# Kernel optimization log

Hardware: AMD Instinct MI355X
Metric: run time of the kernel (lower is better)

## Reference

```python
import jax, jax.numpy as jnp
import numpy as np

WIN = 7            # skimage default win_size
K1 = 0.01
K2 = 0.03
DATA_RANGE = 1.0   # images are in [0, 1]
PAD = (WIN - 1) // 2


def _uniform_filter_valid(x):
    # x: [N, 1, H, W] -> valid 7x7 box filter (== skimage uniform_filter cropped by PAD)
    k = jnp.ones((1, 1, WIN, WIN), x.dtype) / (WIN * WIN)
    return jax.lax.conv_general_dilated(
        x, k, window_strides=(1, 1), padding='VALID',
        dimension_numbers=('NCHW', 'OIHW', 'NCHW'))


def _ssim_mean(a, b):
    # a, b: [B, C, H, W]; each [H, W] slice is one independent SSIM image
    B, C, H, W = a.shape
    x = a.reshape(B * C, 1, H, W)
    y = b.reshape(B * C, 1, H, W)

    ux = _uniform_filter_valid(x)
    uy = _uniform_filter_valid(y)
    uxx = _uniform_filter_valid(x * x)
    uyy = _uniform_filter_valid(y * y)
    uxy = _uniform_filter_valid(x * y)

    NP = WIN * WIN
    cov_norm = NP / (NP - 1.0)  # sample covariance correction (skimage default)
    vx = cov_norm * (uxx - ux * ux)
    vy = cov_norm * (uyy - uy * uy)
    vxy = cov_norm * (uxy - ux * uy)

    C1 = (K1 * DATA_RANGE) ** 2
    C2 = (K2 * DATA_RANGE) ** 2

    S = ((2.0 * ux * uy + C1) * (2.0 * vxy + C2)) / \
        ((ux * ux + uy * uy + C1) * (vx + vy + C2))

    # skimage crops PAD border then means; VALID conv already cropped it.
    # All images are the same size, so np.average(per-image means) == global mean.
    return jnp.mean(S)


def setup_inputs() -> dict:
    key = jax.random.key(0)
    k1, k2 = jax.random.split(key)
    pred = jax.random.uniform(k1, (32, 4, 384, 384), dtype=jnp.float32)
    actual = jax.random.uniform(k2, (32, 4, 384, 384), dtype=jnp.float32)
    return {"pred": pred, "actual": actual}


def reference(pred, actual):
    return _ssim_mean(pred, actual)
```

## Files before the change

kernel.cpp:

```cpp
#include <hip/hip_runtime.h>


#define H 384
#define W 384
#define IMGSZ (H * W)
#define OWIDTH 378
#define NIMG 128
#define NCT 7
#define NRS 6
#define WPI (NCT * NRS)
#define NBLK (NIMG * WPI)
#define P4 65
#define CH 8

__device__ __forceinline__ float wave_reduce(float v) {
#pragma unroll
    for (int off = 32; off > 0; off >>= 1) v += __shfl_down(v, off, 64);
    return v;
}

#define VST(SN, SO, LR, XN, YN) do {                                      \
    const float xo = xv[SO], yo = yv[SO];                                 \
    const float xn = (XN), yn = (YN);                                     \
    sx += xn - xo; sy += yn - yo;                                         \
    sq = fmaf(xn, xn, fmaf(yn, yn, fmaf(-xo, xo, fmaf(-yo, yo, sq))));    \
    sxy = fmaf(xn, yn, fmaf(-xo, yo, sxy));                               \
    xv[SN] = xn; yv[SN] = yn;                                             \
    st[(LR) * P4 + t] = make_float4(sx, sy, sq, sxy);                     \
} while (0)

__global__ __launch_bounds__(64, 4) void ssim_main(const float* __restrict__ pred,
                                                   const float* __restrict__ act,
                                                   float* __restrict__ partials) {
    __shared__ __align__(16) float4 st[CH * P4 + 5];

    const int t = threadIdx.x;
    const int wid = blockIdx.x;
    const int img = wid / WPI;
    const int rem = wid - img * WPI;
    const int rs = rem / NCT;
    const int ct = rem - rs * NCT;

    const int c0 = ct * 58;
    const bool last_rs = (rs == NRS - 1);
    const int y0 = last_rs ? (H - 70) : rs * 64;
    const int ylo = last_rs ? 6 : 0;
    const int nc_raw = OWIDTH - c0;
    const int ncols = (nc_raw < 58) ? nc_raw : 58;

    int col = c0 + t;
    col = (col < W) ? col : (W - 1);
    const float* px = pred + (size_t)img * IMGSZ + (size_t)y0 * W + col;
    const float* py = act  + (size_t)img * IMGSZ + (size_t)y0 * W + col;

    float xv[8], yv[8];
    float pfx[7], pfy[7];
#pragma unroll
    for (int i = 0; i < 7; ++i) { xv[i] = px[i * W]; yv[i] = py[i * W]; }
#pragma unroll
    for (int i = 0; i < 7; ++i) { pfx[i] = px[(7 + i) * W]; pfy[i] = py[(7 + i) * W]; }
    float sx = 0.f, sy = 0.f, sq = 0.f, sxy = 0.f;
#pragma unroll
    for (int i = 0; i < 7; ++i) {
        sx += xv[i]; sy += yv[i];
        sq = fmaf(xv[i], xv[i], fmaf(yv[i], yv[i], sq));
        sxy = fmaf(xv[i], yv[i], sxy);
    }
    st[t] = make_float4(sx, sy, sq, sxy);
    VST(7, 0, 1, pfx[0], pfy[0]);
    VST(0, 1, 2, pfx[1], pfy[1]);
    VST(1, 2, 3, pfx[2], pfy[2]);
    VST(2, 3, 4, pfx[3], pfy[3]);
    VST(3, 4, 5, pfx[4], pfy[4]);
    VST(4, 5, 6, pfx[5], pfy[5]);
    VST(5, 6, 7, pfx[6], pfy[6]);

    const int r = t >> 3;
    const int k = t & 7;
    const int nmax = ncols - 8 * k;
    const float4* qbase = st + r * P4 + 8 * k;
    const float C1B = 0.2401f;
    const float C2B = 2.1168f;
    float acc = 0.f;

    for (int c = 0; c < 8; ++c) {
        float nfx[8], nfy[8];
        if (c < 7) {
#pragma unroll
            for (int i = 0; i < 8; ++i) {
                nfx[i] = px[(8 * c + 14 + i) * W];
                nfy[i] = py[(8 * c + 14 + i) * W];
            }
        }
        float4 q[14];
#pragma unroll
        for (int j = 0; j < 14; ++j) q[j] = qbase[j];
        float Sx  = ((q[0].x + q[1].x) + (q[2].x + q[3].x)) + ((q[4].x + q[5].x) + q[6].x);
        float Sy  = ((q[0].y + q[1].y) + (q[2].y + q[3].y)) + ((q[4].y + q[5].y) + q[6].y);
        float Sq  = ((q[0].z + q[1].z) + (q[2].z + q[3].z)) + ((q[4].z + q[5].z) + q[6].z);
        float Sxy = ((q[0].w + q[1].w) + (q[2].w + q[3].w)) + ((q[4].w + q[5].w) + q[6].w);
        const bool rowok = (8 * c + r) >= ylo;
#pragma unroll
        for (int j = 0; j < 8; ++j) {
            if (j) {
                Sx  += q[j + 6].x - q[j - 1].x;
                Sy  += q[j + 6].y - q[j - 1].y;
                Sq  += q[j + 6].z - q[j - 1].z;
                Sxy += q[j + 6].w - q[j - 1].w;
            }
            const float p  = Sx * Sy;
            const float qq = fmaf(Sx, Sx, Sy * Sy);
            const float n1 = fmaf(2.f, p, C1B);
            const float n2 = fmaf(98.f, Sxy, fmaf(-2.f, p, C2B));
            const float d1 = qq + C1B;
            const float d2 = fmaf(49.f, Sq, C2B - qq);
            const float s  = (n1 * n2) * __builtin_amdgcn_rcpf(d1 * d2);
            acc = (rowok && (j < nmax)) ? acc + s : acc;
        }
        __builtin_amdgcn_sched_barrier(0);
        asm volatile("s_waitcnt lgkmcnt(0)" ::: "memory");
        __builtin_amdgcn_sched_barrier(0);
        if (c < 7) {
            VST(6, 7, 0, nfx[0], nfy[0]);
            VST(7, 0, 1, nfx[1], nfy[1]);
            VST(0, 1, 2, nfx[2], nfy[2]);
            VST(1, 2, 3, nfx[3], nfy[3]);
            VST(2, 3, 4, nfx[4], nfy[4]);
            VST(3, 4, 5, nfx[5], nfy[5]);
            VST(4, 5, 6, nfx[6], nfy[6]);
            VST(5, 6, 7, nfx[7], nfy[7]);
            __builtin_amdgcn_sched_barrier(0);
        }
    }

    const float wsum = wave_reduce(acc);
    if (t == 0) partials[wid] = wsum;
}

__global__ __launch_bounds__(1024) void ssim_finalize(const float* __restrict__ partials,
                                                      float* __restrict__ out) {
    __shared__ double red[1024];
    const int t = threadIdx.x;
    double s = 0.0;
    for (int i = t; i < NBLK; i += 1024) s += (double)partials[i];
    red[t] = s;
    __syncthreads();
#pragma unroll
    for (int off = 512; off > 0; off >>= 1) {
        if (t < off) red[t] += red[t + off];
        __syncthreads();
    }
    if (t == 0) out[0] = (float)(red[0] / ((double)NIMG * OWIDTH * OWIDTH));
}

extern "C" void kernel_launch(void* const* d_in, const int* in_sizes, int n_in,
                              void* d_out, int out_size, void* d_ws, size_t ws_size,
                              hipStream_t stream) {
    const float* pred = (const float*)d_in[0];
    const float* act  = (const float*)d_in[1];
    float* partials = (float*)d_ws;
    ssim_main<<<NBLK, 64, 0, stream>>>(pred, act, partials);
    ssim_finalize<<<1, 1024, 0, stream>>>(partials, (float*)d_out);
}
```

Measured before the change: 172.7 us.

## Replace LDS horizontal window with wave shuffles and retile rows to 63

The horizontal 7-tap box sum moves out of shared memory (LDS float4 staging and lgkmcnt waits) and into cross-lane shuffles (win7), so each lane evaluates SSIM for its own column at every row step. Row strips become 63 output rows each, which removes the special-cased overlapping last strip. Four waves are packed per 256-thread block. In exchange, every lane now does four shuffle-based window sums per row, and lanes near the wave edge compute values that are masked off.

```diff
diff --git a/kernel.cpp b/kernel.cpp
--- a/kernel.cpp
+++ b/kernel.cpp
@@ -6,12 +6,12 @@
 #define IMGSZ (H * W)
 #define OWIDTH 378
 #define NIMG 128
+#define NRS 6
 #define NCT 7
-#define NRS 6
-#define WPI (NCT * NRS)
-#define NBLK (NIMG * WPI)
-#define P4 65
-#define CH 8
+#define WPI (NRS * NCT)
+#define NWAVE (NIMG * WPI)
+#define WVPB 4
+#define NBLKM (NWAVE / WVPB)
 
 __device__ __forceinline__ float wave_reduce(float v) {
 #pragma unroll
@@ -19,122 +19,92 @@
     return v;
 }
 
-#define VST(SN, SO, LR, XN, YN) do {                                      \
-    const float xo = xv[SO], yo = yv[SO];                                 \
-    const float xn = (XN), yn = (YN);                                     \
+__device__ __forceinline__ float win7(float v) {
+    const float a = v + __shfl_down(v, 1, 64);
+    const float b = a + __shfl_down(a, 2, 64);
+    return (b + __shfl_down(a, 4, 64)) + __shfl_down(v, 6, 64);
+}
+
+#define STEP(J, S) do {                                                   \
+    const float xo = xv[S], yo = yv[S];                                   \
+    const float xn = pfx[J], yn = pfy[J];                                 \
     sx += xn - xo; sy += yn - yo;                                         \
     sq = fmaf(xn, xn, fmaf(yn, yn, fmaf(-xo, xo, fmaf(-yo, yo, sq))));    \
     sxy = fmaf(xn, yn, fmaf(-xo, yo, sxy));                               \
-    xv[SN] = xn; yv[SN] = yn;                                             \
-    st[(LR) * P4 + t] = make_float4(sx, sy, sq, sxy);                     \
+    xv[S] = xn; yv[S] = yn;                                               \
+    const float Sx = win7(sx), Sy = win7(sy);                             \
+    const float Sq = win7(sq), Sxy = win7(sxy);                           \
+    const float p  = Sx * Sy;                                             \
+    const float qq = fmaf(Sx, Sx, Sy * Sy);                               \
+    const float n1 = fmaf(2.f, p, C1B);                                   \
+    const float n2 = fmaf(98.f, Sxy, fmaf(-2.f, p, C2B));                 \
+    const float d1 = qq + C1B;                                            \
+    const float d2 = fmaf(49.f, Sq, C2B - qq);                            \
+    const float s  = (n1 * n2) * __builtin_amdgcn_rcpf(d1 * d2);          \
+    acc = lok ? acc + s : acc;                                            \
 } while (0)
 
-__global__ __launch_bounds__(64, 4) void ssim_main(const float* __restrict__ pred,
-                                                   const float* __restrict__ act,
-                                                   float* __restrict__ partials) {
-    __shared__ __align__(16) float4 st[CH * P4 + 5];
+#define BLOCK7 do {                                                       \
+    STEP(0, 6); STEP(1, 0); STEP(2, 1); STEP(3, 2);                       \
+    STEP(4, 3); STEP(5, 4); STEP(6, 5);                                   \
+} while (0)
 
+__global__ __launch_bounds__(256, 5) void ssim_main(const float* __restrict__ pred,
+                                                    const float* __restrict__ act,
+                                                    float* __restrict__ partials) {
     const int t = threadIdx.x;
-    const int wid = blockIdx.x;
+    const int lane = t & 63;
+    const int wid = blockIdx.x * WVPB + (t >> 6);
     const int img = wid / WPI;
     const int rem = wid - img * WPI;
     const int rs = rem / NCT;
     const int ct = rem - rs * NCT;
 
+    const int y0 = rs * 63;
     const int c0 = ct * 58;
-    const bool last_rs = (rs == NRS - 1);
-    const int y0 = last_rs ? (H - 70) : rs * 64;
-    const int ylo = last_rs ? 6 : 0;
     const int nc_raw = OWIDTH - c0;
     const int ncols = (nc_raw < 58) ? nc_raw : 58;
+    const bool lok = lane < ncols;
 
-    int col = c0 + t;
+    int col = c0 + lane;
     col = (col < W) ? col : (W - 1);
     const float* px = pred + (size_t)img * IMGSZ + (size_t)y0 * W + col;
     const float* py = act  + (size_t)img * IMGSZ + (size_t)y0 * W + col;
 
-    float xv[8], yv[8];
-    float pfx[7], pfy[7];
+    const float C1B = 0.2401f;
+    const float C2B = 2.1168f;
+    float acc = 0.f;
+
+    float xv[7], yv[7];
 #pragma unroll
-    for (int i = 0; i < 7; ++i) { xv[i] = px[i * W]; yv[i] = py[i * W]; }
-#pragma unroll
-    for (int i = 0; i < 7; ++i) { pfx[i] = px[(7 + i) * W]; pfy[i] = py[(7 + i) * W]; }
+    for (int i = 0; i < 6; ++i) { xv[i] = px[i * W]; yv[i] = py[i * W]; }
+    xv[6] = 0.f; yv[6] = 0.f;
     float sx = 0.f, sy = 0.f, sq = 0.f, sxy = 0.f;
 #pragma unroll
-    for (int i = 0; i < 7; ++i) {
+    for (int i = 0; i < 6; ++i) {
         sx += xv[i]; sy += yv[i];
         sq = fmaf(xv[i], xv[i], fmaf(yv[i], yv[i], sq));
         sxy = fmaf(xv[i], yv[i], sxy);
     }
-    st[t] = make_float4(sx, sy, sq, sxy);
-    VST(7, 0, 1, pfx[0], pfy[0]);
-    VST(0, 1, 2, pfx[1], pfy[1]);
-    VST(1, 2, 3, pfx[2], pfy[2]);
-    VST(2, 3, 4, pfx[3], pfy[3]);
-    VST(3, 4, 5, pfx[4], pfy[4]);
-    VST(4, 5, 6, pfx[5], pfy[5]);
-    VST(5, 6, 7, pfx[6], pfy[6]);
+    float pfx[7], pfy[7];
+#pragma unroll
+    for (int i = 0; i < 7; ++i) { pfx[i] = px[(6 + i) * W]; pfy[i] = py[(6 + i) * W]; }
 
-    const int r = t >> 3;
-    const int k = t & 7;
-    const int nmax = ncols - 8 * k;
-    const float4* qbase = st + r * P4 + 8 * k;
-    const float C1B = 0.2401f;
-    const float C2B = 2.1168f;
-    float acc = 0.f;
-
+    const float* qx = px + 13 * W;
+    const float* qy = py + 13 * W;
     for (int c = 0; c < 8; ++c) {
-        float nfx[8], nfy[8];
-        if (c < 7) {
+        float nfx[7], nfy[7];
 #pragma unroll
-            for (int i = 0; i < 8; ++i) {
-                nfx[i] = px[(8 * c + 14 + i) * W];
-                nfy[i] = py[(8 * c + 14 + i) * W];
-            }
-        }
-        float4 q[14];
+        for (int i = 0; i < 7; ++i) { nfx[i] = qx[i * W]; nfy[i] = qy[i * W]; }
+        qx += 7 * W; qy += 7 * W;
+        BLOCK7;
 #pragma unroll
-        for (int j = 0; j < 14; ++j) q[j] = qbase[j];
-        float Sx  = ((q[0].x + q[1].x) + (q[2].x + q[3].x)) + ((q[4].x + q[5].x) + q[6].x);
-        float Sy  = ((q[0].y + q[1].y) + (q[2].y + q[3].y)) + ((q[4].y + q[5].y) + q[6].y);
-        float Sq  = ((q[0].z + q[1].z) + (q[2].z + q[3].z)) + ((q[4].z + q[5].z) + q[6].z);
-        float Sxy = ((q[0].w + q[1].w) + (q[2].w + q[3].w)) + ((q[4].w + q[5].w) + q[6].w);
-        const bool rowok = (8 * c + r) >= ylo;
-#pragma unroll
-        for (int j = 0; j < 8; ++j) {
-            if (j) {
-                Sx  += q[j + 6].x - q[j - 1].x;
-                Sy  += q[j + 6].y - q[j - 1].y;
-                Sq  += q[j + 6].z - q[j - 1].z;
-                Sxy += q[j + 6].w - q[j - 1].w;
-            }
-            const float p  = Sx * Sy;
-            const float qq = fmaf(Sx, Sx, Sy * Sy);
-            const float n1 = fmaf(2.f, p, C1B);
-            const float n2 = fmaf(98.f, Sxy, fmaf(-2.f, p, C2B));
-            const float d1 = qq + C1B;
-            const float d2 = fmaf(49.f, Sq, C2B - qq);
-            const float s  = (n1 * n2) * __builtin_amdgcn_rcpf(d1 * d2);
-            acc = (rowok && (j < nmax)) ? acc + s : acc;
-        }
-        __builtin_amdgcn_sched_barrier(0);
-        asm volatile("s_waitcnt lgkmcnt(0)" ::: "memory");
-        __builtin_amdgcn_sched_barrier(0);
-        if (c < 7) {
-            VST(6, 7, 0, nfx[0], nfy[0]);
-            VST(7, 0, 1, nfx[1], nfy[1]);
-            VST(0, 1, 2, nfx[2], nfy[2]);
-            VST(1, 2, 3, nfx[3], nfy[3]);
-            VST(2, 3, 4, nfx[4], nfy[4]);
-            VST(3, 4, 5, nfx[5], nfy[5]);
-            VST(4, 5, 6, nfx[6], nfy[6]);
-            VST(5, 6, 7, nfx[7], nfy[7]);
-            __builtin_amdgcn_sched_barrier(0);
-        }
+        for (int i = 0; i < 7; ++i) { pfx[i] = nfx[i]; pfy[i] = nfy[i]; }
     }
+    BLOCK7;
 
     const float wsum = wave_reduce(acc);
-    if (t == 0) partials[wid] = wsum;
+    if (lane == 0) partials[wid] = wsum;
 }
 
 __global__ __launch_bounds__(1024) void ssim_finalize(const float* __restrict__ partials,
@@ -142,7 +112,7 @@
     __shared__ double red[1024];
     const int t = threadIdx.x;
     double s = 0.0;
-    for (int i = t; i < NBLK; i += 1024) s += (double)partials[i];
+    for (int i = t; i < NWAVE; i += 1024) s += (double)partials[i];
     red[t] = s;
     __syncthreads();
 #pragma unroll
@@ -159,6 +129,6 @@
     const float* pred = (const float*)d_in[0];
     const float* act  = (const float*)d_in[1];
     float* partials = (float*)d_ws;
-    ssim_main<<<NBLK, 64, 0, stream>>>(pred, act, partials);
+    ssim_main<<<NBLKM, 256, 0, stream>>>(pred, act, partials);
     ssim_finalize<<<1, 1024, 0, stream>>>(partials, (float*)d_out);
 }
```

Measured after the change: 190.5 us. 1.1x slower.
